# Performance work log

Hardware: AMD Instinct MI355X
Metric: run time of the kernel (lower is better)

Reference implementation:

```python
import jax, jax.numpy as jnp
import numpy as np

EPS = 1e-08
STRIDE = 1


def setup_inputs() -> dict:
    key = jax.random.key(0)
    k_x, k_s, k_sw, k_w = jax.random.split(key, 4)
    B, Cin, Cout, D = 8, 32, 32, 48
    style_size, K = 2, 3
    x = jax.random.normal(k_x, (B, Cin, D, D, D), dtype=jnp.float32)
    s = jax.random.normal(k_s, (B, style_size), dtype=jnp.float32)
    # lecun_normal-style scaling for params
    style_weight = jax.random.normal(k_sw, (Cin, style_size), dtype=jnp.float32) / np.sqrt(style_size)
    style_bias = jnp.ones((Cin,), dtype=jnp.float32)
    weight = jax.random.normal(k_w, (Cout, Cin, K, K, K), dtype=jnp.float32) / np.sqrt(Cin * K * K * K)
    bias = jnp.zeros((Cout,), dtype=jnp.float32)
    return {"x": x, "s": s, "style_weight": style_weight,
            "style_bias": style_bias, "weight": weight, "bias": bias}


def reference(x, s, style_weight, style_bias, weight, bias):
    # Style modulation: per-sample per-input-channel scale  (B, Cin)
    s_mod = jnp.dot(s, style_weight.T) + style_bias
    # Modulated weights: (B, Cout, Cin, K, K, K)
    w = weight[None] * s_mod[:, None, :, None, None, None]
    # Demodulation over (Cin, K, K, K) per (B, Cout)
    norm = jnp.sqrt(jnp.sum(w ** 2, axis=(2, 3, 4, 5), keepdims=True) + jnp.float32(EPS))
    w_n = w / norm

    def single_conv(x_i, w_i):
        # x_i: (Cin, D, H, W), w_i: (Cout, Cin, K, K, K)
        out = jax.lax.conv_general_dilated(
            lhs=x_i[None], rhs=w_i,
            window_strides=(STRIDE,) * 3, padding='VALID',
            dimension_numbers=('NCDHW', 'OIDHW', 'NCDHW'))
        return out[0]

    y = jax.vmap(single_conv)(x, w_n)  # (B, Cout, D', H', W')
    return y + bias[None, :, None, None, None]
```

## Files before the change

kernel.cpp:

```cpp
#include <hip/hip_runtime.h>


typedef unsigned short u16;
typedef __bf16 bf16x8 __attribute__((ext_vector_type(8)));
typedef u16 u16x8 __attribute__((ext_vector_type(8)));
typedef float f32x4 __attribute__((ext_vector_type(4)));

#define CHUNKB   (110592 * 16)
#define XT_BYTES (32u * CHUNKB)
#define WA_ELEMS (8 * 4 * 32 * 28 * 8)

__device__ __forceinline__ u16 f2bf(float f) {
    __bf16 h = (__bf16)f;
    return __builtin_bit_cast(u16, h);
}

__device__ __forceinline__ void dma16(const void* g, void* l) {
    __builtin_amdgcn_global_load_lds(
        (const __attribute__((address_space(1))) unsigned*)g,
        (__attribute__((address_space(3))) unsigned*)l, 16, 0, 0);
}

__global__ __launch_bounds__(256) void xpose_kernel(
    const float* __restrict__ x, u16* __restrict__ xT)
{
    int gid = blockIdx.x * 256 + threadIdx.x;
    int quad = gid % 27648;
    int bc   = gid / 27648;
    int site0 = quad * 4;
    const float* xp = x + (size_t)bc * 8 * 110592 + site0;
    float4 v[8];
#pragma unroll
    for (int j = 0; j < 8; ++j) v[j] = *(const float4*)(xp + (size_t)j * 110592);
    u16* op = xT + (size_t)gid * 32;
#pragma unroll
    for (int k = 0; k < 4; ++k) {
        u16x8 o;
#pragma unroll
        for (int j = 0; j < 8; ++j) o[j] = f2bf(((const float*)&v[j])[k]);
        *(u16x8*)(op + k * 8) = o;
    }
}

__global__ __launch_bounds__(64) void wnorm8_kernel(
    const float* __restrict__ s, const float* __restrict__ sw,
    const float* __restrict__ sb, const float* __restrict__ w,
    u16* __restrict__ wA)
{
    int bc = blockIdx.x;
    int b = bc >> 5, co = bc & 31;
    int lane = threadIdx.x;
    float s0 = s[2 * b], s1 = s[2 * b + 1];

    float sum = 0.f;
    for (int i = lane; i < 864; i += 64) {
        int ci = i / 27;
        float m = fmaf(s0, sw[2 * ci], fmaf(s1, sw[2 * ci + 1], sb[ci]));
        float v = w[co * 864 + i] * m;
        sum += v * v;
    }
#pragma unroll
    for (int off = 32; off; off >>= 1) sum += __shfl_xor(sum, off, 64);
    float rn = 1.0f / sqrtf(sum + 1e-8f);

    for (int i = lane; i < 864; i += 64) {
        int ci = i / 27, tap = i - ci * 27;
        float m = fmaf(s0, sw[2 * ci], fmaf(s1, sw[2 * ci + 1], sb[ci]));
        float v = w[co * 864 + i] * m * rn;
        int chunk = ci >> 3, ci8 = ci & 7;
        wA[(((b * 4 + chunk) * 32 + co) * 28 + tap) * 8 + ci8] = f2bf(v);
    }
    if (lane < 32) {
        int c = lane >> 3, ci8 = lane & 7;
        wA[(((b * 4 + c) * 32 + co) * 28 + 27) * 8 + ci8] = 0;
    }
}

__global__ __launch_bounds__(512, 4) void conv_dma(
    const u16* __restrict__ xT, const u16* __restrict__ wA,
    const float* __restrict__ bias, float* __restrict__ out)
{
    __shared__ u16 sx[2][16384];

    int blk = blockIdx.x;
    int zt = blk % 12, yt = (blk / 12) % 12, b = blk / 144;
    int z0 = zt * 4, y0 = yt * 4;

    int t = threadIdx.x;
    int l = t & 63, w = t >> 6;
    int ln = l & 15;
    int tq = l >> 4;
    int zw = w & 3, yp = w >> 2;

    int bbase[7];
#pragma unroll
    for (int s = 0; s < 7; ++s) {
        int tap = 4 * s + tq; if (tap > 26) tap = 26;
        int dz = tap / 9, rr = tap - dz * 9;
        int dy = rr / 3, dx = rr - dy * 3;
        bbase[s] = ((zw + dz) * 300 + (2 * yp + dy) * 50 + ln + dx) * 16;
    }
    int aoff = (ln * 28 + tq) * 16;

    f32x4 acc[2][3][2];
#pragma unroll
    for (int i = 0; i < 2; i++)
#pragma unroll
        for (int j = 0; j < 3; j++)
#pragma unroll
            for (int h = 0; h < 2; h++) acc[i][j][h] = (f32x4)0.f;

    u16x8 A0r[7], A1r[7];

    const char* xc = (const char*)xT + (size_t)(b * 4) * CHUNKB;

#define ISSUE(c, d) { \
    _Pragma("unroll") \
    for (int i = 0; i < 4; ++i) { \
        int sidx = t + i * 512; \
        int z = sidx / 300, r_ = sidx - z * 300; \
        int y = r_ / 50, x = r_ - y * 50; \
        long o = ((long)((z0 + z) * 48 + (y0 + y)) * 48 + x) * 16; \
        long mx = (long)CHUNKB - 16; \
        size_t go = (size_t)(o < mx ? o : mx); \
        dma16(xc + (size_t)(c) * CHUNKB + go, \
              (char*)&sx[d][0] + (size_t)(i * 512 + w * 64) * 16); } }

#define PREA(c) { \
    const char* wB = (const char*)(wA + (size_t)(b * 4 + (c)) * (32 * 28 * 8)); \
    _Pragma("unroll") \
    for (int s = 0; s < 7; ++s) { \
        A0r[s] = *(const u16x8*)(wB + aoff + s * 64); \
        A1r[s] = *(const u16x8*)(wB + aoff + 7168 + s * 64); } }

#define COMPUTE(d) { \
    const char* sb_ = (const char*)&sx[d][0]; \
    _Pragma("unroll") \
    for (int s = 0; s < 7; ++s) { \
        __builtin_amdgcn_s_setprio(1); \
        _Pragma("unroll") \
        for (int yr = 0; yr < 2; ++yr) { \
            const char* p = sb_ + bbase[s] + yr * 800; \
            _Pragma("unroll") \
            for (int xt = 0; xt < 3; ++xt) { \
                bf16x8 Bf = *(const bf16x8*)(p + xt * 256); \
                acc[yr][xt][0] = __builtin_amdgcn_mfma_f32_16x16x32_bf16( \
                    __builtin_bit_cast(bf16x8, A0r[s]), Bf, acc[yr][xt][0], 0, 0, 0); \
                acc[yr][xt][1] = __builtin_amdgcn_mfma_f32_16x16x32_bf16( \
                    __builtin_bit_cast(bf16x8, A1r[s]), Bf, acc[yr][xt][1], 0, 0, 0); \
            } \
        } \
        __builtin_amdgcn_s_setprio(0); \
    } }

    ISSUE(0, 0)
    __syncthreads();
    PREA(0)
    ISSUE(1, 1)
    COMPUTE(0)
    __syncthreads();
    PREA(1)
    ISSUE(2, 0)
    COMPUTE(1)
    __syncthreads();
    PREA(2)
    ISSUE(3, 1)
    COMPUTE(0 + 0)
    __syncthreads();
    PREA(3)
    COMPUTE(1)

    int oz = z0 + zw;
    if (oz < 46) {
#pragma unroll
        for (int yr = 0; yr < 2; ++yr) {
            int oy = y0 + 2 * yp + yr;
            if (oy >= 46) continue;
#pragma unroll
            for (int xt = 0; xt < 3; ++xt) {
                int ox = xt * 16 + ln;
                if (ox >= 46) continue;
#pragma unroll
                for (int h = 0; h < 2; ++h) {
                    f32x4 a = acc[yr][xt][h];
#pragma unroll
                    for (int r = 0; r < 4; ++r) {
                        int co = h * 16 + tq * 4 + r;
                        out[(size_t)(b * 32 + co) * 97336 + oz * 2116 + oy * 46 + ox]
                            = a[r] + bias[co];
                    }
                }
            }
        }
    }
#undef ISSUE
#undef PREA
#undef COMPUTE
}

__global__ __launch_bounds__(64) void wnorm16_kernel(
    const float* __restrict__ s, const float* __restrict__ sw,
    const float* __restrict__ sb, const float* __restrict__ w,
    u16* __restrict__ wA)
{
    int bc = blockIdx.x;
    int b = bc >> 5, co = bc & 31;
    int lane = threadIdx.x;
    float s0 = s[2 * b], s1 = s[2 * b + 1];

    float sum = 0.f;
    for (int i = lane; i < 864; i += 64) {
        int ci = i / 27;
        float m = fmaf(s0, sw[2 * ci], fmaf(s1, sw[2 * ci + 1], sb[ci]));
        float v = w[co * 864 + i] * m;
        sum += v * v;
    }
#pragma unroll
    for (int off = 32; off; off >>= 1) sum += __shfl_xor(sum, off, 64);
    float rn = 1.0f / sqrtf(sum + 1e-8f);

    for (int i = lane; i < 864; i += 64) {
        int ci = i / 27, tap = i - ci * 27;
        float m = fmaf(s0, sw[2 * ci], fmaf(s1, sw[2 * ci + 1], sb[ci]));
        float v = w[co * 864 + i] * m * rn;
        int chunk = ci >> 4, ci16 = ci & 15;
        wA[(((b * 2 + chunk) * 32 + co) * 28 + tap) * 16 + ci16] = f2bf(v);
    }
    if (lane < 32) {
        int c = lane >> 4, ci16 = lane & 15;
        wA[(((b * 2 + c) * 32 + co) * 28 + 27) * 16 + ci16] = 0;
    }
}

__global__ __launch_bounds__(512) void conv_fallback(
    const float* __restrict__ xin, const u16* __restrict__ wA,
    const float* __restrict__ bias, float* __restrict__ out)
{
    __shared__ u16 sx[28800];

    int blk = blockIdx.x;
    int zt = blk % 12, yt = (blk / 12) % 12, b = blk / 144;
    int z0 = zt * 4, y0 = yt * 4;

    int t = threadIdx.x;
    int l = t & 63, w = t >> 6;
    int ln = l & 15, ch = (l >> 4) & 1, tp = l >> 5, rg = l >> 4;
    int zw = w & 3, yp = w >> 2;

    f32x4 acc[2][3][2];
#pragma unroll
    for (int i = 0; i < 2; i++)
#pragma unroll
        for (int j = 0; j < 3; j++)
#pragma unroll
            for (int h = 0; h < 2; h++) acc[i][j][h] = (f32x4)0.f;

    for (int chunk = 0; chunk < 2; ++chunk) {
        __syncthreads();
        for (int idx = t; idx < 3600; idx += 512) {
            int x = idx % 50;
            int r = idx / 50;
            int cg = r & 1; r >>= 1;
            int y = r % 6, z = r / 6;
            int gz = z0 + z, gy = y0 + y;
            bool inb = (x < 48) && (gy < 48) && (gz < 48);
            const float* xp = xin + (size_t)(b * 32 + chunk * 16 + cg * 8) * 110592
                              + gz * 2304 + gy * 48 + x;
            u16x8 v;
#pragma unroll
            for (int j = 0; j < 8; j++) {
                float f = inb ? xp[(size_t)j * 110592] : 0.f;
                v[j] = f2bf(f);
            }
            *(u16x8*)&sx[idx * 8] = v;
        }
        __syncthreads();

        const u16* wAc = wA + (b * 2 + chunk) * (32 * 28 * 16);
        int aoff = (ln * 28 + tp) * 16 + ch * 8;

#pragma unroll
        for (int s = 0; s < 14; ++s) {
            int tapA = 2 * s + tp;
            bf16x8 A0 = __builtin_bit_cast(bf16x8, *(const u16x8*)(wAc + aoff + s * 32));
            bf16x8 A1 = __builtin_bit_cast(bf16x8, *(const u16x8*)(wAc + aoff + 16 * 28 * 16 + s * 32));
            int tapB = tapA > 26 ? 26 : tapA;
            int dz = tapB / 9;
            int rr = tapB - dz * 9;
            int dy = rr / 3;
            int dx = rr - dy * 3;
            int zr = zw + dz;
#pragma unroll
            for (int yr = 0; yr < 2; ++yr) {
                int yy = 2 * yp + yr + dy;
                int eb = (((zr * 6 + yy) * 2 + ch) * 50 + ln + dx) * 8;
#pragma unroll
                for (int xt = 0; xt < 3; ++xt) {
                    bf16x8 Bf = __builtin_bit_cast(bf16x8, *(const u16x8*)&sx[eb + xt * 128]);
                    acc[yr][xt][0] = __builtin_amdgcn_mfma_f32_16x16x32_bf16(A0, Bf, acc[yr][xt][0], 0, 0, 0);
                    acc[yr][xt][1] = __builtin_amdgcn_mfma_f32_16x16x32_bf16(A1, Bf, acc[yr][xt][1], 0, 0, 0);
                }
            }
        }
    }

    int oz = z0 + zw;
    if (oz < 46) {
#pragma unroll
        for (int yr = 0; yr < 2; ++yr) {
            int oy = y0 + 2 * yp + yr;
            if (oy >= 46) continue;
#pragma unroll
            for (int xt = 0; xt < 3; ++xt) {
                int ox = xt * 16 + ln;
                if (ox >= 46) continue;
#pragma unroll
                for (int h = 0; h < 2; ++h) {
                    f32x4 a = acc[yr][xt][h];
#pragma unroll
                    for (int r = 0; r < 4; ++r) {
                        int co = h * 16 + rg * 4 + r;
                        out[(size_t)(b * 32 + co) * 97336 + oz * 2116 + oy * 46 + ox]
                            = a[r] + bias[co];
                    }
                }
            }
        }
    }
}

extern "C" void kernel_launch(void* const* d_in, const int* in_sizes, int n_in,
                              void* d_out, int out_size, void* d_ws, size_t ws_size,
                              hipStream_t stream) {
    const float* x    = (const float*)d_in[0];
    const float* s    = (const float*)d_in[1];
    const float* sw   = (const float*)d_in[2];
    const float* sb   = (const float*)d_in[3];
    const float* wgt  = (const float*)d_in[4];
    const float* bias = (const float*)d_in[5];
    float* out = (float*)d_out;

    const size_t need = (size_t)XT_BYTES + WA_ELEMS * sizeof(u16);
    if (ws_size >= need) {
        u16* xT = (u16*)d_ws;
        u16* wA = (u16*)((char*)d_ws + XT_BYTES);
        hipLaunchKernelGGL(xpose_kernel, dim3(3456), dim3(256), 0, stream, x, xT);
        hipLaunchKernelGGL(wnorm8_kernel, dim3(256), dim3(64), 0, stream,
                           s, sw, sb, wgt, wA);
        hipLaunchKernelGGL(conv_dma, dim3(12 * 12 * 8), dim3(512), 0, stream,
                           xT, wA, bias, out);
    } else {
        u16* wA = (u16*)d_ws;
        hipLaunchKernelGGL(wnorm16_kernel, dim3(256), dim3(64), 0, stream,
                           s, sw, sb, wgt, wA);
        hipLaunchKernelGGL(conv_fallback, dim3(12 * 12 * 8), dim3(512), 0, stream,
                           x, wA, bias, out);
    }
}
```

Before: 115.9 us.

## Software-pipeline LDS/weight reads with MFMAs and remap block order across batches

The compute stage now double-buffers fragments: the LDS B-fragments and global A-weights for step s+1 are loaded while the MFMAs for step s run. This replaces the old pattern of preloading all seven A-weight pairs per chunk and then interleaving LDS reads inside the MFMA loop. It also drops the s_setprio hints and remaps blockIdx so consecutive blocks come from different batch samples. The aim is to hide LDS and global latency, cut register pressure from 14 preloaded A vectors, and spread L2 traffic, but the global A loads now sit inside the compute stage.

```diff
diff --git a/kernel.cpp b/kernel.cpp
--- a/kernel.cpp
+++ b/kernel.cpp
@@ -82,7 +82,9 @@
 {
     __shared__ u16 sx[2][16384];
 
-    int blk = blockIdx.x;
+    int orig = blockIdx.x;
+    int blk = (orig & 7) * 144 + (orig >> 3);
+
     int zt = blk % 12, yt = (blk / 12) % 12, b = blk / 144;
     int z0 = zt * 4, y0 = yt * 4;
 
@@ -109,8 +111,6 @@
         for (int j = 0; j < 3; j++)
 #pragma unroll
             for (int h = 0; h < 2; h++) acc[i][j][h] = (f32x4)0.f;
-
-    u16x8 A0r[7], A1r[7];
 
     const char* xc = (const char*)xT + (size_t)(b * 4) * CHUNKB;
 
@@ -126,49 +126,66 @@
         dma16(xc + (size_t)(c) * CHUNKB + go, \
               (char*)&sx[d][0] + (size_t)(i * 512 + w * 64) * 16); } }
 
-#define PREA(c) { \
+#define BREAD(p0, p1, p2, p3, p4, p5, sidx) { \
+    const char* p = sb_ + bbase[sidx]; \
+    p0 = *(const u16x8*)(p); \
+    p1 = *(const u16x8*)(p + 256); \
+    p2 = *(const u16x8*)(p + 512); \
+    p3 = *(const u16x8*)(p + 800); \
+    p4 = *(const u16x8*)(p + 800 + 256); \
+    p5 = *(const u16x8*)(p + 800 + 512); }
+
+#define AREAD(A0, A1, sidx) { \
+    A0 = *(const u16x8*)(wB + aoff + (sidx) * 64); \
+    A1 = *(const u16x8*)(wB + aoff + 7168 + (sidx) * 64); }
+
+#define MFMA6(A0, A1, f0, f1, f2, f3, f4, f5) { \
+    acc[0][0][0] = __builtin_amdgcn_mfma_f32_16x16x32_bf16(__builtin_bit_cast(bf16x8, A0), __builtin_bit_cast(bf16x8, f0), acc[0][0][0], 0, 0, 0); \
+    acc[0][0][1] = __builtin_amdgcn_mfma_f32_16x16x32_bf16(__builtin_bit_cast(bf16x8, A1), __builtin_bit_cast(bf16x8, f0), acc[0][0][1], 0, 0, 0); \
+    acc[0][1][0] = __builtin_amdgcn_mfma_f32_16x16x32_bf16(__builtin_bit_cast(bf16x8, A0), __builtin_bit_cast(bf16x8, f1), acc[0][1][0], 0, 0, 0); \
+    acc[0][1][1] = __builtin_amdgcn_mfma_f32_16x16x32_bf16(__builtin_bit_cast(bf16x8, A1), __builtin_bit_cast(bf16x8, f1), acc[0][1][1], 0, 0, 0); \
+    acc[0][2][0] = __builtin_amdgcn_mfma_f32_16x16x32_bf16(__builtin_bit_cast(bf16x8, A0), __builtin_bit_cast(bf16x8, f2), acc[0][2][0], 0, 0, 0); \
+    acc[0][2][1] = __builtin_amdgcn_mfma_f32_16x16x32_bf16(__builtin_bit_cast(bf16x8, A1), __builtin_bit_cast(bf16x8, f2), acc[0][2][1], 0, 0, 0); \
+    acc[1][0][0] = __builtin_amdgcn_mfma_f32_16x16x32_bf16(__builtin_bit_cast(bf16x8, A0), __builtin_bit_cast(bf16x8, f3), acc[1][0][0], 0, 0, 0); \
+    acc[1][0][1] = __builtin_amdgcn_mfma_f32_16x16x32_bf16(__builtin_bit_cast(bf16x8, A1), __builtin_bit_cast(bf16x8, f3), acc[1][0][1], 0, 0, 0); \
+    acc[1][1][0] = __builtin_amdgcn_mfma_f32_16x16x32_bf16(__builtin_bit_cast(bf16x8, A0), __builtin_bit_cast(bf16x8, f4), acc[1][1][0], 0, 0, 0); \
+    acc[1][1][1] = __builtin_amdgcn_mfma_f32_16x16x32_bf16(__builtin_bit_cast(bf16x8, A1), __builtin_bit_cast(bf16x8, f4), acc[1][1][1], 0, 0, 0); \
+    acc[1][2][0] = __builtin_amdgcn_mfma_f32_16x16x32_bf16(__builtin_bit_cast(bf16x8, A0), __builtin_bit_cast(bf16x8, f5), acc[1][2][0], 0, 0, 0); \
+    acc[1][2][1] = __builtin_amdgcn_mfma_f32_16x16x32_bf16(__builtin_bit_cast(bf16x8, A1), __builtin_bit_cast(bf16x8, f5), acc[1][2][1], 0, 0, 0); }
+
+#define COMPUTE(c, d) { \
     const char* wB = (const char*)(wA + (size_t)(b * 4 + (c)) * (32 * 28 * 8)); \
-    _Pragma("unroll") \
-    for (int s = 0; s < 7; ++s) { \
-        A0r[s] = *(const u16x8*)(wB + aoff + s * 64); \
-        A1r[s] = *(const u16x8*)(wB + aoff + 7168 + s * 64); } }
-
-#define COMPUTE(d) { \
     const char* sb_ = (const char*)&sx[d][0]; \
-    _Pragma("unroll") \
-    for (int s = 0; s < 7; ++s) { \
-        __builtin_amdgcn_s_setprio(1); \
-        _Pragma("unroll") \
-        for (int yr = 0; yr < 2; ++yr) { \
-            const char* p = sb_ + bbase[s] + yr * 800; \
-            _Pragma("unroll") \
-            for (int xt = 0; xt < 3; ++xt) { \
-                bf16x8 Bf = *(const bf16x8*)(p + xt * 256); \
-                acc[yr][xt][0] = __builtin_amdgcn_mfma_f32_16x16x32_bf16( \
-                    __builtin_bit_cast(bf16x8, A0r[s]), Bf, acc[yr][xt][0], 0, 0, 0); \
-                acc[yr][xt][1] = __builtin_amdgcn_mfma_f32_16x16x32_bf16( \
-                    __builtin_bit_cast(bf16x8, A1r[s]), Bf, acc[yr][xt][1], 0, 0, 0); \
-            } \
-        } \
-        __builtin_amdgcn_s_setprio(0); \
-    } }
+    u16x8 fa0, fa1, fa2, fa3, fa4, fa5, fb0, fb1, fb2, fb3, fb4, fb5; \
+    u16x8 Aa0, Aa1, Ab0, Ab1; \
+    BREAD(fa0, fa1, fa2, fa3, fa4, fa5, 0) \
+    AREAD(Aa0, Aa1, 0) \
+     BREAD(fb0, fb1, fb2, fb3, fb4, fb5, 1) AREAD(Ab0, Ab1, 1) \
+              MFMA6(Aa0, Aa1, fa0, fa1, fa2, fa3, fa4, fa5) \
+     BREAD(fa0, fa1, fa2, fa3, fa4, fa5, 2) AREAD(Aa0, Aa1, 2) \
+              MFMA6(Ab0, Ab1, fb0, fb1, fb2, fb3, fb4, fb5) \
+     BREAD(fb0, fb1, fb2, fb3, fb4, fb5, 3) AREAD(Ab0, Ab1, 3) \
+              MFMA6(Aa0, Aa1, fa0, fa1, fa2, fa3, fa4, fa5) \
+     BREAD(fa0, fa1, fa2, fa3, fa4, fa5, 4) AREAD(Aa0, Aa1, 4) \
+              MFMA6(Ab0, Ab1, fb0, fb1, fb2, fb3, fb4, fb5) \
+     BREAD(fb0, fb1, fb2, fb3, fb4, fb5, 5) AREAD(Ab0, Ab1, 5) \
+              MFMA6(Aa0, Aa1, fa0, fa1, fa2, fa3, fa4, fa5) \
+     BREAD(fa0, fa1, fa2, fa3, fa4, fa5, 6) AREAD(Aa0, Aa1, 6) \
+              MFMA6(Ab0, Ab1, fb0, fb1, fb2, fb3, fb4, fb5) \
+     MFMA6(Aa0, Aa1, fa0, fa1, fa2, fa3, fa4, fa5) }
 
     ISSUE(0, 0)
     __syncthreads();
-    PREA(0)
     ISSUE(1, 1)
-    COMPUTE(0)
+    COMPUTE(0, 0)
     __syncthreads();
-    PREA(1)
     ISSUE(2, 0)
-    COMPUTE(1)
+    COMPUTE(1, 1)
     __syncthreads();
-    PREA(2)
     ISSUE(3, 1)
-    COMPUTE(0 + 0)
+    COMPUTE(2, 0)
     __syncthreads();
-    PREA(3)
-    COMPUTE(1)
+    COMPUTE(3, 1)
 
     int oz = z0 + zw;
     if (oz < 46) {
@@ -194,7 +211,9 @@
         }
     }
 #undef ISSUE
-#undef PREA
+#undef BREAD
+#undef AREAD
+#undef MFMA6
 #undef COMPUTE
 }
 
```

Result: faster. 105.5 us (-9.0%).
